# Kernel tuning notes

Hardware: AMD Instinct MI355X
Metric: run time of the kernel (lower is better)

## Reference

```python
import jax, jax.numpy as jnp
import numpy as np

N = 100000      # nodes (cells)
E = 1600000     # edges (kNN graph, avg degree 16)
DIM_IN = 128    # input features per cell
H = 8           # heads
C1 = 8          # per-head channels, layer 1 (concat -> 64)
DIM_OUT = 10    # classes (concat=False -> mean over heads)
NEG_SLOPE = 0.2


def setup_inputs() -> dict:
    key = jax.random.key(0)
    ks = jax.random.split(key, 10)
    s = 0.1
    return {
        "x": jax.random.normal(ks[0], (N, DIM_IN), dtype=jnp.float32),
        "edge_index": jax.random.randint(ks[1], (2, E), 0, N, dtype=jnp.int64),
        "W1": jax.random.normal(ks[2], (DIM_IN, H * C1), dtype=jnp.float32) * s,
        "a_src1": jax.random.normal(ks[3], (H, C1), dtype=jnp.float32) * s,
        "a_dst1": jax.random.normal(ks[4], (H, C1), dtype=jnp.float32) * s,
        "b1": jnp.zeros((H * C1,), dtype=jnp.float32),
        "W2": jax.random.normal(ks[5], (H * C1, H * DIM_OUT), dtype=jnp.float32) * s,
        "a_src2": jax.random.normal(ks[6], (H, DIM_OUT), dtype=jnp.float32) * s,
        "a_dst2": jax.random.normal(ks[7], (H, DIM_OUT), dtype=jnp.float32) * s,
        "b2": jnp.zeros((DIM_OUT,), dtype=jnp.float32),
    }


def _gat_layer(x, src, dst, W, a_src, a_dst, bias, concat, n):
    """PyG-style GATConv: gather -> edge attention -> segment softmax -> scatter."""
    h_, c_ = a_src.shape
    h = (x @ W).reshape(n, h_, c_)                       # [N, H, C]
    alpha_s = jnp.einsum('nhc,hc->nh', h, a_src)         # [N, H]
    alpha_d = jnp.einsum('nhc,hc->nh', h, a_dst)         # [N, H]
    # per-edge logits; PyG: message from src j to dst i, softmax over dst
    e = jax.nn.leaky_relu(alpha_s[src] + alpha_d[dst], NEG_SLOPE)  # [E, H]
    e_max = jax.ops.segment_max(e, dst, num_segments=n)            # [N, H]
    e = jnp.exp(e - e_max[dst])
    denom = jax.ops.segment_sum(e, dst, num_segments=n)            # [N, H]
    alpha = e / denom[dst]                                          # [E, H]
    msg = h[src] * alpha[:, :, None]                                # [E, H, C]
    out = jax.ops.segment_sum(msg, dst, num_segments=n)             # [N, H, C]
    out = out.reshape(n, h_ * c_) if concat else out.mean(axis=1)
    return out + bias


def reference(x, edge_index, W1, a_src1, a_dst1, b1, W2, a_src2, a_dst2, b2):
    n = x.shape[0]
    loops = jnp.arange(n, dtype=edge_index.dtype)
    src = jnp.concatenate([edge_index[0], loops])  # PyG adds self-loops by default
    dst = jnp.concatenate([edge_index[1], loops])
    h = _gat_layer(x, src, dst, W1, a_src1, a_dst1, b1, True, n)   # [N, 64]
    h = jax.nn.elu(h)
    h = _gat_layer(h, src, dst, W2, a_src2, a_dst2, b2, False, n)  # [N, dim_out]
    return jax.nn.log_softmax(h, axis=1)
```

## Files before the change

### kernel.cpp

```cpp
#include <hip/hip_runtime.h>
#include <hip/hip_bf16.h>
#include <cstdint>

#define CAP 64
#define SLICES 8
#define CHUNK_EDGES 2048

__device__ __forceinline__ float lrelu(float v) { return fmaxf(v, 0.2f * v); }

typedef float f32x2 __attribute__((ext_vector_type(2)));
__device__ __forceinline__ float2 q2f(unsigned short u) {
    f32x2 v = __builtin_amdgcn_cvt_pk_f32_fp8((int)u, false);
    return make_float2(v.x, v.y);
}
__device__ __forceinline__ int f2q4(float a, float b, float c, float d) {
    int p = __builtin_amdgcn_cvt_pk_fp8_f32(a, b, 0, false);
    p = __builtin_amdgcn_cvt_pk_fp8_f32(c, d, p, true);
    return p;
}
__device__ __forceinline__ float b2f(unsigned short u) { return __uint_as_float(((unsigned)u) << 16); }
__device__ __forceinline__ unsigned short f2b(float f) {
    unsigned u = __float_as_uint(f);
    return (unsigned short)((u + 0x7FFFu + ((u >> 16) & 1u)) >> 16);
}

__global__ __launch_bounds__(256, 4) void k_bg(const int* __restrict__ ei, int E, int N,
                                               int* __restrict__ cnt, int* __restrict__ bucket,
                                               const float* __restrict__ x,
                                               const float* __restrict__ W,
                                               const float* __restrict__ asrc,
                                               const float* __restrict__ adst,
                                               unsigned char* __restrict__ h1q,
                                               float* __restrict__ als, float* __restrict__ ald,
                                               int buildBlocks) {
    __shared__ unsigned short xs[64 * 132];
    if ((int)blockIdx.x < buildBlocks) {
        const int s = blockIdx.x & (SLICES - 1);
        const int chunk = blockIdx.x >> 3;
        const int sliceN = (N + SLICES - 1) / SLICES;
        const int lo = s * sliceN;
        const int hi = min(N, lo + sliceN);
        const int base = chunk * CHUNK_EDGES;
        if (base + CHUNK_EDGES <= E) {
            const int e0 = base + (int)threadIdx.x * 4;
            const int e1 = e0 + 1024;
            int4 d0 = *(const int4*)(ei + E + e0);
            int4 s0 = *(const int4*)(ei + e0);
            int4 d1 = *(const int4*)(ei + E + e1);
            int4 s1 = *(const int4*)(ei + e1);
            int a0 = -1, a1 = -1, a2 = -1, a3 = -1, a4 = -1, a5 = -1, a6 = -1, a7 = -1;
            if (d0.x >= lo && d0.x < hi) a0 = atomicAdd(&cnt[d0.x], 1);
            if (d0.y >= lo && d0.y < hi) a1 = atomicAdd(&cnt[d0.y], 1);
            if (d0.z >= lo && d0.z < hi) a2 = atomicAdd(&cnt[d0.z], 1);
            if (d0.w >= lo && d0.w < hi) a3 = atomicAdd(&cnt[d0.w], 1);
            if (d1.x >= lo && d1.x < hi) a4 = atomicAdd(&cnt[d1.x], 1);
            if (d1.y >= lo && d1.y < hi) a5 = atomicAdd(&cnt[d1.y], 1);
            if (d1.z >= lo && d1.z < hi) a6 = atomicAdd(&cnt[d1.z], 1);
            if (d1.w >= lo && d1.w < hi) a7 = atomicAdd(&cnt[d1.w], 1);
            if (a0 >= 0 && a0 < CAP) bucket[(size_t)d0.x * CAP + a0] = s0.x;
            if (a1 >= 0 && a1 < CAP) bucket[(size_t)d0.y * CAP + a1] = s0.y;
            if (a2 >= 0 && a2 < CAP) bucket[(size_t)d0.z * CAP + a2] = s0.z;
            if (a3 >= 0 && a3 < CAP) bucket[(size_t)d0.w * CAP + a3] = s0.w;
            if (a4 >= 0 && a4 < CAP) bucket[(size_t)d1.x * CAP + a4] = s1.x;
            if (a5 >= 0 && a5 < CAP) bucket[(size_t)d1.y * CAP + a5] = s1.y;
            if (a6 >= 0 && a6 < CAP) bucket[(size_t)d1.z * CAP + a6] = s1.z;
            if (a7 >= 0 && a7 < CAP) bucket[(size_t)d1.w * CAP + a7] = s1.w;
        } else {
            const int end = E;
            for (int e = base + (int)threadIdx.x; e < end; e += 256) {
                int d = ei[E + e];
                if (d >= lo && d < hi) {
                    int a = atomicAdd(&cnt[d], 1);
                    if (a < CAP) bucket[(size_t)d * CAP + a] = ei[e];
                }
            }
        }
        return;
    }
    const int t = threadIdx.x;
    const int rowBase = ((int)blockIdx.x - buildBlocks) * 64;
#pragma unroll
    for (int i = 0; i < 8; ++i) {
        int g = i * 256 + t;
        int r = g >> 5, c4 = (g & 31) << 2;
        float4 v = make_float4(0.f, 0.f, 0.f, 0.f);
        int row = rowBase + r;
        if (row < N) v = *(const float4*)(x + (size_t)row * 128 + c4);
        ushort4 u;
        u.x = f2b(v.x); u.y = f2b(v.y); u.z = f2b(v.z); u.w = f2b(v.w);
        *(ushort4*)(&xs[r * 132 + c4]) = u;
    }
    __syncthreads();
    const int tx = t & 15;
    const int ty = t >> 4;
    float acc[4][4] = {};
#pragma unroll 2
    for (int kc = 0; kc < 32; ++kc) {
        float a_[4][4];
#pragma unroll
        for (int i = 0; i < 4; ++i) {
            ushort4 u = *(const ushort4*)(&xs[(4 * ty + i) * 132 + kc * 4]);
            a_[i][0] = b2f(u.x); a_[i][1] = b2f(u.y); a_[i][2] = b2f(u.z); a_[i][3] = b2f(u.w);
        }
        float4 w[4];
#pragma unroll
        for (int kk = 0; kk < 4; ++kk) w[kk] = *(const float4*)(W + (size_t)(kc * 4 + kk) * 64 + tx * 4);
#pragma unroll
        for (int i = 0; i < 4; ++i) {
#pragma unroll
            for (int j = 0; j < 4; ++j) {
                acc[i][j] += a_[i][0] * ((const float*)&w[0])[j]
                           + a_[i][1] * ((const float*)&w[1])[j]
                           + a_[i][2] * ((const float*)&w[2])[j]
                           + a_[i][3] * ((const float*)&w[3])[j];
            }
        }
    }
    const int h = tx >> 1;
    float4 av = *(const float4*)(asrc + tx * 4);
    float4 dv = *(const float4*)(adst + tx * 4);
#pragma unroll
    for (int i = 0; i < 4; ++i) {
        int row = rowBase + 4 * ty + i;
        float ps = acc[i][0] * av.x + acc[i][1] * av.y + acc[i][2] * av.z + acc[i][3] * av.w;
        float pd = acc[i][0] * dv.x + acc[i][1] * dv.y + acc[i][2] * dv.z + acc[i][3] * dv.w;
        ps += __shfl_xor(ps, 1);
        pd += __shfl_xor(pd, 1);
        if (row < N) {
            *(int*)(h1q + (size_t)row * 64 + tx * 4) = f2q4(acc[i][0], acc[i][1], acc[i][2], acc[i][3]);
            if ((tx & 1) == 0) {
                als[(size_t)row * 8 + h] = ps;
                ald[(size_t)row * 8 + h] = pd;
            }
        }
    }
}

__global__ __launch_bounds__(256) void k_gemm2(const float* __restrict__ hin,
                                               const float* __restrict__ W,
                                               const float* __restrict__ asrc,
                                               const float* __restrict__ adst,
                                               unsigned char* __restrict__ h2q,
                                               float* __restrict__ ald, int N) {
    __shared__ float xs[64 * 68];
    __shared__ float wt[80 * 68];
    const int t = threadIdx.x;
    const int rowBase = blockIdx.x * 64;
#pragma unroll
    for (int i = 0; i < 4; ++i) {
        int g = i * 256 + t;
        int r = g >> 4, c4 = (g & 15) << 2;
        float4 v = make_float4(0.f, 0.f, 0.f, 0.f);
        int row = rowBase + r;
        if (row < N) v = *(const float4*)(hin + (size_t)row * 64 + c4);
        *(float4*)(&xs[r * 68 + c4]) = v;
    }
#pragma unroll
    for (int i = 0; i < 20; ++i) {
        int g = i * 256 + t;
        int k = g / 80, c = g % 80;
        wt[c * 68 + k] = W[g];
    }
    __syncthreads();
    const int tx = t & 15;
    const int ty = t >> 4;
    float acc[4][5] = {};
#pragma unroll 4
    for (int kc = 0; kc < 16; ++kc) {
        float4 a[4];
#pragma unroll
        for (int i = 0; i < 4; ++i) a[i] = *(const float4*)(&xs[(4 * ty + i) * 68 + kc * 4]);
        float4 w[5];
#pragma unroll
        for (int j = 0; j < 5; ++j) w[j] = *(const float4*)(&wt[(5 * tx + j) * 68 + kc * 4]);
#pragma unroll
        for (int i = 0; i < 4; ++i) {
#pragma unroll
            for (int j = 0; j < 5; ++j) {
                acc[i][j] += a[i].x * w[j].x + a[i].y * w[j].y + a[i].z * w[j].z + a[i].w * w[j].w;
            }
        }
    }
    const int h = tx >> 1;
    float a2[5], d2[5];
#pragma unroll
    for (int j = 0; j < 5; ++j) { a2[j] = asrc[tx * 5 + j]; d2[j] = adst[tx * 5 + j]; }
    __syncthreads();
    unsigned char* qs = (unsigned char*)xs;
#pragma unroll
    for (int i = 0; i < 4; ++i) {
        int row = rowBase + 4 * ty + i;
        float ps = 0.f, pd = 0.f;
#pragma unroll
        for (int j = 0; j < 5; ++j) { ps += acc[i][j] * a2[j]; pd += acc[i][j] * d2[j]; }
        ps += __shfl_xor(ps, 1);
        pd += __shfl_xor(pd, 1);
        int p0 = __builtin_amdgcn_cvt_pk_fp8_f32(acc[i][0], acc[i][1], 0, false);
        int p1 = __builtin_amdgcn_cvt_pk_fp8_f32(acc[i][2], acc[i][3], 0, false);
        int p2 = __builtin_amdgcn_cvt_pk_fp8_f32(acc[i][4], acc[i][4], 0, false);
        unsigned char* q = qs + (4 * ty + i) * 96 + h * 12 + (tx & 1) * 5;
        q[0] = (unsigned char)(p0 & 0xFF);
        q[1] = (unsigned char)((p0 >> 8) & 0xFF);
        q[2] = (unsigned char)(p1 & 0xFF);
        q[3] = (unsigned char)((p1 >> 8) & 0xFF);
        q[4] = (unsigned char)(p2 & 0xFF);
        if ((tx & 1) == 0) {
            *(unsigned short*)(qs + (size_t)(4 * ty + i) * 96 + h * 12 + 10) = f2b(ps);
            if (row < N) ald[(size_t)row * 8 + h] = pd;
        }
    }
    __syncthreads();
    for (int g = t; g < 1536; g += 256) {
        int row = g / 24;
        if (rowBase + row < N)
            *(unsigned int*)(h2q + (size_t)rowBase * 96 + (size_t)g * 4) = ((unsigned int*)qs)[g];
    }
}

__global__ __launch_bounds__(256) void k_agg1(const int* __restrict__ cnt, const int* __restrict__ bucket,
                                              const unsigned char* __restrict__ h1q,
                                              const float* __restrict__ als, const float* __restrict__ ald,
                                              const float* __restrict__ b1,
                                              float* __restrict__ helu, int N) {
    int w = threadIdx.x >> 6, lane = threadIdx.x & 63;
    int e = lane >> 3, h = lane & 7;
    int n = blockIdx.x * 4 + w;
    bool act = n < N;
    float acc[8] = {};
    float den = 0.f;
    if (act) {
        float aldh = ald[(size_t)n * 8 + h];
        auto body = [&](int m0, int m1, float a_s) {
            float wl = __expf(lrelu(a_s + aldh));
            den += wl;
            f32x2 v;
            v = __builtin_amdgcn_cvt_pk_f32_fp8(m0, false); acc[0] += wl * v.x; acc[1] += wl * v.y;
            v = __builtin_amdgcn_cvt_pk_f32_fp8(m0, true);  acc[2] += wl * v.x; acc[3] += wl * v.y;
            v = __builtin_amdgcn_cvt_pk_f32_fp8(m1, false); acc[4] += wl * v.x; acc[5] += wl * v.y;
            v = __builtin_amdgcn_cvt_pk_f32_fp8(m1, true);  acc[6] += wl * v.x; acc[7] += wl * v.y;
        };
        if (e == 0) {
            const unsigned char* r = h1q + (size_t)n * 64 + h * 8;
            body(*(const int*)r, *(const int*)(r + 4), als[(size_t)n * 8 + h]);
        }
        int k = min(cnt[n], CAP);
        const int* bp = bucket + (size_t)n * CAP;
        int i = e;
        while (i + 8 < k) {
            int s0 = bp[i], s1 = bp[i + 8];
            const unsigned char* r0 = h1q + (size_t)s0 * 64 + h * 8;
            const unsigned char* r1 = h1q + (size_t)s1 * 64 + h * 8;
            int m00 = *(const int*)r0, m01 = *(const int*)(r0 + 4);
            int m10 = *(const int*)r1, m11 = *(const int*)(r1 + 4);
            float as0 = als[(size_t)s0 * 8 + h];
            float as1 = als[(size_t)s1 * 8 + h];
            body(m00, m01, as0);
            body(m10, m11, as1);
            i += 16;
        }
        if (i < k) {
            int s0 = bp[i];
            const unsigned char* r0 = h1q + (size_t)s0 * 64 + h * 8;
            body(*(const int*)r0, *(const int*)(r0 + 4), als[(size_t)s0 * 8 + h]);
        }
    }
#pragma unroll
    for (int off = 8; off < 64; off <<= 1) {
        den += __shfl_xor(den, off);
#pragma unroll
        for (int j = 0; j < 8; ++j) acc[j] += __shfl_xor(acc[j], off);
    }
    if (act && e == 0) {
        float inv = 1.f / den;
        float o[8];
#pragma unroll
        for (int j = 0; j < 8; ++j) {
            float v = acc[j] * inv + b1[h * 8 + j];
            o[j] = v > 0.f ? v : __expf(v) - 1.f;
        }
        *(float4*)(helu + (size_t)n * 64 + h * 8)     = make_float4(o[0], o[1], o[2], o[3]);
        *(float4*)(helu + (size_t)n * 64 + h * 8 + 4) = make_float4(o[4], o[5], o[6], o[7]);
    }
}

__global__ __launch_bounds__(256) void k_agg2(const int* __restrict__ cnt, const int* __restrict__ bucket,
                                              const unsigned char* __restrict__ h2q,
                                              const float* __restrict__ ald,
                                              const float* __restrict__ b2,
                                              float* __restrict__ out, int N) {
    __shared__ float sm[4][80];
    int w = threadIdx.x >> 6, lane = threadIdx.x & 63;
    int e = lane >> 3, h = lane & 7;
    int n = blockIdx.x * 4 + w;
    bool act = n < N;
    float acc[10] = {};
    float den = 0.f;
    if (act) {
        float aldh = ald[(size_t)n * 8 + h];
        auto body = [&](int m0, int m1, int m2) {
            float a_s = b2f((unsigned short)(((unsigned)m2) >> 16));
            float wl = __expf(lrelu(a_s + aldh));
            den += wl;
            f32x2 v;
            v = __builtin_amdgcn_cvt_pk_f32_fp8(m0, false); acc[0] += wl * v.x; acc[1] += wl * v.y;
            v = __builtin_amdgcn_cvt_pk_f32_fp8(m0, true);  acc[2] += wl * v.x; acc[3] += wl * v.y;
            v = __builtin_amdgcn_cvt_pk_f32_fp8(m1, false); acc[4] += wl * v.x; acc[5] += wl * v.y;
            v = __builtin_amdgcn_cvt_pk_f32_fp8(m1, true);  acc[6] += wl * v.x; acc[7] += wl * v.y;
            v = __builtin_amdgcn_cvt_pk_f32_fp8(m2, false); acc[8] += wl * v.x; acc[9] += wl * v.y;
        };
        if (e == 0) {
            const unsigned char* r = h2q + (size_t)n * 96 + h * 12;
            body(*(const int*)r, *(const int*)(r + 4), *(const int*)(r + 8));
        }
        int k = min(cnt[n], CAP);
        const int* bp = bucket + (size_t)n * CAP;
        int i = e;
        while (i + 8 < k) {
            int s0 = bp[i], s1 = bp[i + 8];
            const unsigned char* r0 = h2q + (size_t)s0 * 96 + h * 12;
            const unsigned char* r1 = h2q + (size_t)s1 * 96 + h * 12;
            int m00 = *(const int*)r0, m01 = *(const int*)(r0 + 4), m02 = *(const int*)(r0 + 8);
            int m10 = *(const int*)r1, m11 = *(const int*)(r1 + 4), m12 = *(const int*)(r1 + 8);
            body(m00, m01, m02);
            body(m10, m11, m12);
            i += 16;
        }
        if (i < k) {
            int s0 = bp[i];
            const unsigned char* r0 = h2q + (size_t)s0 * 96 + h * 12;
            body(*(const int*)r0, *(const int*)(r0 + 4), *(const int*)(r0 + 8));
        }
    }
#pragma unroll
    for (int off = 8; off < 64; off <<= 1) {
        den += __shfl_xor(den, off);
#pragma unroll
        for (int j = 0; j < 10; ++j) acc[j] += __shfl_xor(acc[j], off);
    }
    if (act && e == 0) {
        float inv = 1.f / den;
#pragma unroll
        for (int j = 0; j < 10; ++j) sm[w][h * 10 + j] = acc[j] * inv;
    }
    __syncthreads();
    float m = 0.f;
    if (act && lane < 10) {
#pragma unroll
        for (int hh = 0; hh < 8; ++hh) m += sm[w][hh * 10 + lane];
        m = m * 0.125f + b2[lane];
    }
    __syncthreads();
    if (act && lane < 10) sm[w][lane] = m;
    __syncthreads();
    if (act && lane < 10) {
        float mx = -1e30f;
#pragma unroll
        for (int c = 0; c < 10; ++c) mx = fmaxf(mx, sm[w][c]);
        float ssum = 0.f;
#pragma unroll
        for (int c = 0; c < 10; ++c) ssum += __expf(sm[w][c] - mx);
        out[(size_t)n * 10 + lane] = m - mx - __logf(ssum);
    }
}

extern "C" void kernel_launch(void* const* d_in, const int* in_sizes, int n_in,
                              void* d_out, int out_size, void* d_ws, size_t ws_size,
                              hipStream_t stream) {
    const float* x     = (const float*)d_in[0];
    const int*   ei    = (const int*)d_in[1];
    const float* W1    = (const float*)d_in[2];
    const float* asrc1 = (const float*)d_in[3];
    const float* adst1 = (const float*)d_in[4];
    const float* b1    = (const float*)d_in[5];
    const float* W2    = (const float*)d_in[6];
    const float* asrc2 = (const float*)d_in[7];
    const float* adst2 = (const float*)d_in[8];
    const float* b2    = (const float*)d_in[9];
    float* out = (float*)d_out;

    int N = in_sizes[0] / 128;
    int E = in_sizes[1] / 2;

    char* base = (char*)d_ws;
    size_t off = 0;
    auto alloc = [&](size_t bytes) {
        char* p = base + off;
        off = (off + bytes + 255) & ~(size_t)255;
        return p;
    };
    int*            cnt    = (int*)alloc((size_t)N * 4);
    int*            bucket = (int*)alloc((size_t)N * CAP * 4);
    float*          helu   = (float*)alloc((size_t)N * 64 * 4);
    unsigned char*  hq     = (unsigned char*)alloc((size_t)N * 96);
    float*          als    = (float*)alloc((size_t)N * 8 * 4);
    float*          ald    = (float*)alloc((size_t)N * 8 * 4);
    (void)ws_size; (void)n_in; (void)out_size;

    (void)hipMemsetAsync(cnt, 0, (size_t)N * 4, stream);
    int chunks = (E + CHUNK_EDGES - 1) / CHUNK_EDGES;
    int buildBlocks = chunks * SLICES;
    int gemmBlocks = (N + 63) / 64;
    k_bg<<<buildBlocks + gemmBlocks, 256, 0, stream>>>(ei, E, N, cnt, bucket,
                                                       x, W1, asrc1, adst1, hq, als, ald, buildBlocks);
    k_agg1<<<(N + 3) / 4, 256, 0, stream>>>(cnt, bucket, hq, als, ald, b1, helu, N);
    k_gemm2<<<(N + 63) / 64, 256, 0, stream>>>(helu, W2, asrc2, adst2, hq, ald, N);
    k_agg2<<<(N + 3) / 4, 256, 0, stream>>>(cnt, bucket, hq, ald, b2, out, N);
}
```

Before: 348.6 us.

## Map eight threads per node in aggregation kernels with serial prefetched edge loop

```diff
diff --git a/kernel.cpp b/kernel.cpp
--- a/kernel.cpp
+++ b/kernel.cpp
@@ -222,65 +222,53 @@
                                               const float* __restrict__ als, const float* __restrict__ ald,
                                               const float* __restrict__ b1,
                                               float* __restrict__ helu, int N) {
-    int w = threadIdx.x >> 6, lane = threadIdx.x & 63;
-    int e = lane >> 3, h = lane & 7;
-    int n = blockIdx.x * 4 + w;
-    bool act = n < N;
+    const int t = threadIdx.x;
+    const int n = blockIdx.x * 32 + (t >> 3);
+    const int h = t & 7;
+    if (n >= N) return;
     float acc[8] = {};
     float den = 0.f;
-    if (act) {
-        float aldh = ald[(size_t)n * 8 + h];
-        auto body = [&](int m0, int m1, float a_s) {
-            float wl = __expf(lrelu(a_s + aldh));
-            den += wl;
-            f32x2 v;
-            v = __builtin_amdgcn_cvt_pk_f32_fp8(m0, false); acc[0] += wl * v.x; acc[1] += wl * v.y;
-            v = __builtin_amdgcn_cvt_pk_f32_fp8(m0, true);  acc[2] += wl * v.x; acc[3] += wl * v.y;
-            v = __builtin_amdgcn_cvt_pk_f32_fp8(m1, false); acc[4] += wl * v.x; acc[5] += wl * v.y;
-            v = __builtin_amdgcn_cvt_pk_f32_fp8(m1, true);  acc[6] += wl * v.x; acc[7] += wl * v.y;
-        };
-        if (e == 0) {
-            const unsigned char* r = h1q + (size_t)n * 64 + h * 8;
-            body(*(const int*)r, *(const int*)(r + 4), als[(size_t)n * 8 + h]);
-        }
-        int k = min(cnt[n], CAP);
-        const int* bp = bucket + (size_t)n * CAP;
-        int i = e;
-        while (i + 8 < k) {
-            int s0 = bp[i], s1 = bp[i + 8];
-            const unsigned char* r0 = h1q + (size_t)s0 * 64 + h * 8;
-            const unsigned char* r1 = h1q + (size_t)s1 * 64 + h * 8;
-            int m00 = *(const int*)r0, m01 = *(const int*)(r0 + 4);
-            int m10 = *(const int*)r1, m11 = *(const int*)(r1 + 4);
-            float as0 = als[(size_t)s0 * 8 + h];
-            float as1 = als[(size_t)s1 * 8 + h];
-            body(m00, m01, as0);
-            body(m10, m11, as1);
-            i += 16;
-        }
-        if (i < k) {
-            int s0 = bp[i];
-            const unsigned char* r0 = h1q + (size_t)s0 * 64 + h * 8;
-            body(*(const int*)r0, *(const int*)(r0 + 4), als[(size_t)s0 * 8 + h]);
-        }
-    }
-#pragma unroll
-    for (int off = 8; off < 64; off <<= 1) {
-        den += __shfl_xor(den, off);
-#pragma unroll
-        for (int j = 0; j < 8; ++j) acc[j] += __shfl_xor(acc[j], off);
-    }
-    if (act && e == 0) {
-        float inv = 1.f / den;
-        float o[8];
-#pragma unroll
-        for (int j = 0; j < 8; ++j) {
-            float v = acc[j] * inv + b1[h * 8 + j];
-            o[j] = v > 0.f ? v : __expf(v) - 1.f;
-        }
-        *(float4*)(helu + (size_t)n * 64 + h * 8)     = make_float4(o[0], o[1], o[2], o[3]);
-        *(float4*)(helu + (size_t)n * 64 + h * 8 + 4) = make_float4(o[4], o[5], o[6], o[7]);
-    }
+    const float aldh = ald[(size_t)n * 8 + h];
+    auto body = [&](int m0, int m1, float a_s) {
+        float wl = __expf(lrelu(a_s + aldh));
+        den += wl;
+        f32x2 v;
+        v = __builtin_amdgcn_cvt_pk_f32_fp8(m0, false); acc[0] += wl * v.x; acc[1] += wl * v.y;
+        v = __builtin_amdgcn_cvt_pk_f32_fp8(m0, true);  acc[2] += wl * v.x; acc[3] += wl * v.y;
+        v = __builtin_amdgcn_cvt_pk_f32_fp8(m1, false); acc[4] += wl * v.x; acc[5] += wl * v.y;
+        v = __builtin_amdgcn_cvt_pk_f32_fp8(m1, true);  acc[6] += wl * v.x; acc[7] += wl * v.y;
+    };
+    {
+        const unsigned char* r = h1q + (size_t)n * 64 + h * 8;
+        body(*(const int*)r, *(const int*)(r + 4), als[(size_t)n * 8 + h]);
+    }
+    const int k = min(cnt[n], CAP);
+    const int* bp = bucket + (size_t)n * CAP;
+    if (k > 0) {
+        int s = bp[0];
+        const unsigned char* r = h1q + (size_t)s * 64 + h * 8;
+        int m0 = *(const int*)r, m1 = *(const int*)(r + 4);
+        float as = als[(size_t)s * 8 + h];
+        for (int i = 0; i < k; ++i) {
+            int c0 = m0, c1 = m1; float cs = as;
+            if (i + 1 < k) {
+                int s2 = bp[i + 1];
+                const unsigned char* r2 = h1q + (size_t)s2 * 64 + h * 8;
+                m0 = *(const int*)r2; m1 = *(const int*)(r2 + 4);
+                as = als[(size_t)s2 * 8 + h];
+            }
+            body(c0, c1, cs);
+        }
+    }
+    float inv = 1.f / den;
+    float o[8];
+#pragma unroll
+    for (int j = 0; j < 8; ++j) {
+        float v = acc[j] * inv + b1[h * 8 + j];
+        o[j] = v > 0.f ? v : __expf(v) - 1.f;
+    }
+    *(float4*)(helu + (size_t)n * 64 + h * 8)     = make_float4(o[0], o[1], o[2], o[3]);
+    *(float4*)(helu + (size_t)n * 64 + h * 8 + 4) = make_float4(o[4], o[5], o[6], o[7]);
 }
 
 __global__ __launch_bounds__(256) void k_agg2(const int* __restrict__ cnt, const int* __restrict__ bucket,
@@ -288,78 +276,65 @@
                                               const float* __restrict__ ald,
                                               const float* __restrict__ b2,
                                               float* __restrict__ out, int N) {
-    __shared__ float sm[4][80];
-    int w = threadIdx.x >> 6, lane = threadIdx.x & 63;
-    int e = lane >> 3, h = lane & 7;
-    int n = blockIdx.x * 4 + w;
-    bool act = n < N;
+    const int t = threadIdx.x;
+    const int n = blockIdx.x * 32 + (t >> 3);
+    const int h = t & 7;
+    if (n >= N) return;
     float acc[10] = {};
     float den = 0.f;
-    if (act) {
-        float aldh = ald[(size_t)n * 8 + h];
-        auto body = [&](int m0, int m1, int m2) {
-            float a_s = b2f((unsigned short)(((unsigned)m2) >> 16));
-            float wl = __expf(lrelu(a_s + aldh));
-            den += wl;
-            f32x2 v;
-            v = __builtin_amdgcn_cvt_pk_f32_fp8(m0, false); acc[0] += wl * v.x; acc[1] += wl * v.y;
-            v = __builtin_amdgcn_cvt_pk_f32_fp8(m0, true);  acc[2] += wl * v.x; acc[3] += wl * v.y;
-            v = __builtin_amdgcn_cvt_pk_f32_fp8(m1, false); acc[4] += wl * v.x; acc[5] += wl * v.y;
-            v = __builtin_amdgcn_cvt_pk_f32_fp8(m1, true);  acc[6] += wl * v.x; acc[7] += wl * v.y;
-            v = __builtin_amdgcn_cvt_pk_f32_fp8(m2, false); acc[8] += wl * v.x; acc[9] += wl * v.y;
-        };
-        if (e == 0) {
-            const unsigned char* r = h2q + (size_t)n * 96 + h * 12;
-            body(*(const int*)r, *(const int*)(r + 4), *(const int*)(r + 8));
-        }
-        int k = min(cnt[n], CAP);
-        const int* bp = bucket + (size_t)n * CAP;
-        int i = e;
-        while (i + 8 < k) {
-            int s0 = bp[i], s1 = bp[i + 8];
-            const unsigned char* r0 = h2q + (size_t)s0 * 96 + h * 12;
-            const unsigned char* r1 = h2q + (size_t)s1 * 96 + h * 12;
-            int m00 = *(const int*)r0, m01 = *(const int*)(r0 + 4), m02 = *(const int*)(r0 + 8);
-            int m10 = *(const int*)r1, m11 = *(const int*)(r1 + 4), m12 = *(const int*)(r1 + 8);
-            body(m00, m01, m02);
-            body(m10, m11, m12);
-            i += 16;
-        }
-        if (i < k) {
-            int s0 = bp[i];
-            const unsigned char* r0 = h2q + (size_t)s0 * 96 + h * 12;
-            body(*(const int*)r0, *(const int*)(r0 + 4), *(const int*)(r0 + 8));
-        }
-    }
-#pragma unroll
-    for (int off = 8; off < 64; off <<= 1) {
-        den += __shfl_xor(den, off);
+    const float aldh = ald[(size_t)n * 8 + h];
+    auto body = [&](int m0, int m1, int m2) {
+        float a_s = b2f((unsigned short)(((unsigned)m2) >> 16));
+        float wl = __expf(lrelu(a_s + aldh));
+        den += wl;
+        f32x2 v;
+        v = __builtin_amdgcn_cvt_pk_f32_fp8(m0, false); acc[0] += wl * v.x; acc[1] += wl * v.y;
+        v = __builtin_amdgcn_cvt_pk_f32_fp8(m0, true);  acc[2] += wl * v.x; acc[3] += wl * v.y;
+        v = __builtin_amdgcn_cvt_pk_f32_fp8(m1, false); acc[4] += wl * v.x; acc[5] += wl * v.y;
+        v = __builtin_amdgcn_cvt_pk_f32_fp8(m1, true);  acc[6] += wl * v.x; acc[7] += wl * v.y;
+        v = __builtin_amdgcn_cvt_pk_f32_fp8(m2, false); acc[8] += wl * v.x; acc[9] += wl * v.y;
+    };
+    {
+        const unsigned char* r = h2q + (size_t)n * 96 + h * 12;
+        body(*(const int*)r, *(const int*)(r + 4), *(const int*)(r + 8));
+    }
+    const int k = min(cnt[n], CAP);
+    const int* bp = bucket + (size_t)n * CAP;
+    if (k > 0) {
+        int s = bp[0];
+        const unsigned char* r = h2q + (size_t)s * 96 + h * 12;
+        int m0 = *(const int*)r, m1 = *(const int*)(r + 4), m2 = *(const int*)(r + 8);
+        for (int i = 0; i < k; ++i) {
+            int c0 = m0, c1 = m1, c2 = m2;
+            if (i + 1 < k) {
+                int s2 = bp[i + 1];
+                const unsigned char* r2 = h2q + (size_t)s2 * 96 + h * 12;
+                m0 = *(const int*)r2; m1 = *(const int*)(r2 + 4); m2 = *(const int*)(r2 + 8);
+            }
+            body(c0, c1, c2);
+        }
+    }
+    float inv = 1.f / den;
+#pragma unroll
+    for (int j = 0; j < 10; ++j) acc[j] *= inv;
+#pragma unroll
+    for (int off = 1; off < 8; off <<= 1) {
 #pragma unroll
         for (int j = 0; j < 10; ++j) acc[j] += __shfl_xor(acc[j], off);
     }
-    if (act && e == 0) {
-        float inv = 1.f / den;
-#pragma unroll
-        for (int j = 0; j < 10; ++j) sm[w][h * 10 + j] = acc[j] * inv;
-    }
-    __syncthreads();
-    float m = 0.f;
-    if (act && lane < 10) {
-#pragma unroll
-        for (int hh = 0; hh < 8; ++hh) m += sm[w][hh * 10 + lane];
-        m = m * 0.125f + b2[lane];
-    }
-    __syncthreads();
-    if (act && lane < 10) sm[w][lane] = m;
-    __syncthreads();
-    if (act && lane < 10) {
+    if (h == 0) {
+        float m[10];
+#pragma unroll
+        for (int j = 0; j < 10; ++j) m[j] = acc[j] * 0.125f + b2[j];
         float mx = -1e30f;
 #pragma unroll
-        for (int c = 0; c < 10; ++c) mx = fmaxf(mx, sm[w][c]);
+        for (int j = 0; j < 10; ++j) mx = fmaxf(mx, m[j]);
         float ssum = 0.f;
 #pragma unroll
-        for (int c = 0; c < 10; ++c) ssum += __expf(sm[w][c] - mx);
-        out[(size_t)n * 10 + lane] = m - mx - __logf(ssum);
+        for (int j = 0; j < 10; ++j) ssum += __expf(m[j] - mx);
+        float lg = __logf(ssum);
+#pragma unroll
+        for (int j = 0; j < 10; ++j) out[(size_t)n * 10 + j] = m[j] - mx - lg;
     }
 }
 
@@ -402,7 +377,7 @@
     int gemmBlocks = (N + 63) / 64;
     k_bg<<<buildBlocks + gemmBlocks, 256, 0, stream>>>(ei, E, N, cnt, bucket,
                                                        x, W1, asrc1, adst1, hq, als, ald, buildBlocks);
-    k_agg1<<<(N + 3) / 4, 256, 0, stream>>>(cnt, bucket, hq, als, ald, b1, helu, N);
+    k_agg1<<<(N + 31) / 32, 256, 0, stream>>>(cnt, bucket, hq, als, ald, b1, helu, N);
     k_gemm2<<<(N + 63) / 64, 256, 0, stream>>>(helu, W2, asrc2, adst2, hq, ald, N);
-    k_agg2<<<(N + 3) / 4, 256, 0, stream>>>(cnt, bucket, hq, ald, b2, out, N);
-}
+    k_agg2<<<(N + 31) / 32, 256, 0, stream>>>(cnt, bucket, hq, ald, b2, out, N);
+}
```

Result: no change. 343.3 us (-1.5%).
